# Optimization experiments

Measured on AMD Instinct MI355X. Metric: run time of the kernel, lower is better.

Reference implementation:

```python
import jax, jax.numpy as jnp
import numpy as np

N, E, H = 50000, 800000, 128
HQ = H // 4  # 32


def _mlp(x, w1, b1, w2, b2):
    return jax.nn.relu(x @ w1 + b1) @ w2 + b2


def setup_inputs() -> dict:
    key = jax.random.key(0)
    ks = jax.random.split(key, 16)

    def lin(k, fan_in, fan_out):
        lim = 1.0 / np.sqrt(fan_in)
        kw, kb = jax.random.split(k)
        w = jax.random.uniform(kw, (fan_in, fan_out), jnp.float32, -lim, lim)
        b = jax.random.uniform(kb, (fan_out,), jnp.float32, -lim, lim)
        return w, b

    x = jax.random.normal(ks[0], (N, H), jnp.float32)
    pos = jax.random.normal(ks[1], (N, 3), jnp.float32)
    edge_index = jax.random.randint(ks[2], (2, E), 0, N, jnp.int64)

    pw1, pb1 = lin(ks[3], 3, HQ)
    pw2, pb2 = lin(ks[4], HQ, HQ)
    mw1, mb1 = lin(ks[5], 2 * H + HQ, H)
    mw2, mb2 = lin(ks[6], H, H)
    uw1, ub1 = lin(ks[7], 2 * H, H)
    uw2, ub2 = lin(ks[8], H, H)

    return dict(x=x, pos=pos, edge_index=edge_index,
                pw1=pw1, pb1=pb1, pw2=pw2, pb2=pb2,
                mw1=mw1, mb1=mb1, mw2=mw2, mb2=mb2,
                uw1=uw1, ub1=ub1, uw2=uw2, ub2=ub2)


def reference(x, pos, edge_index,
              pw1, pb1, pw2, pb2,
              mw1, mb1, mw2, mb2,
              uw1, ub1, uw2, ub2):
    row, col = edge_index[0], edge_index[1]
    # position features from relative positions [E, 3] -> [E, H//4]
    pos_feat = _mlp(pos[row] - pos[col], pw1, pb1, pw2, pb2)
    # per-edge messages [E, 2H + H//4] -> [E, H]
    msg_in = jnp.concatenate([x[row], x[col], pos_feat], axis=-1)
    messages = _mlp(msg_in, mw1, mb1, mw2, mb2)
    # scatter-add messages into destination nodes (index_add on col)
    agg = jax.ops.segment_sum(messages, col, num_segments=x.shape[0])
    # node update [N, 2H] -> [N, H]
    return _mlp(jnp.concatenate([x, agg], axis=-1), uw1, ub1, uw2, ub2)
```

## Files before the change

### kernel.cpp

```cpp
#include <hip/hip_runtime.h>
#include <hip/hip_bf16.h>

#define NN 50000
#define NE 800000
#define HD 128
#define SCAN_CHUNK 1024
#define SCAN_BLOCKS ((NN + SCAN_CHUNK - 1) / SCAN_CHUNK)

typedef __attribute__((ext_vector_type(8))) short s16x8;
typedef __attribute__((ext_vector_type(4))) float f32x4;

static __device__ __forceinline__ unsigned short f2bf(float f) {
    unsigned int u = __float_as_uint(f);
    u = (u + 0x7FFFu + ((u >> 16) & 1u)) >> 16;
    return (unsigned short)u;
}
static __device__ __forceinline__ float bf2f(unsigned short h) {
    return __uint_as_float(((unsigned int)h) << 16);
}
static __device__ __forceinline__ unsigned int f2bf2(float lo, float hi) {
    __hip_bfloat162 h = __float22bfloat162_rn(make_float2(lo, hi));
    return *reinterpret_cast<unsigned int*>(&h);
}

#define WFENCE() do { asm volatile("s_waitcnt lgkmcnt(0)" ::: "memory"); \
                      __builtin_amdgcn_sched_barrier(0); } while (0)

__global__ void prep_kernel(const float* __restrict__ pw2, const float* __restrict__ pb2,
                            const float* __restrict__ mw1, const float* __restrict__ mb1,
                            float* __restrict__ Wpc, float* __restrict__ bc)
{
    int tid = threadIdx.x;
    for (int idx = tid; idx < 32 * 128; idx += 256) {
        int j = idx >> 7, k = idx & 127;
        float s = 0.f;
        #pragma unroll 8
        for (int i = 0; i < 32; ++i) s += pw2[j * 32 + i] * mw1[(256 + i) * 128 + k];
        Wpc[idx] = s;
    }
    if (tid < 128) {
        float s = mb1[tid];
        #pragma unroll 8
        for (int i = 0; i < 32; ++i) s += pb2[i] * mw1[(256 + i) * 128 + tid];
        bc[tid] = s;
    }
}

__global__ void prep2_kernel(const float* __restrict__ mw2, const float* __restrict__ mb2,
                             const float* __restrict__ uw1,
                             float* __restrict__ W3, float* __restrict__ b3)
{
    int idx = blockIdx.x * 256 + threadIdx.x;
    if (idx < 128 * 128) {
        int k = idx >> 7, j = idx & 127;
        float s = 0.f;
        #pragma unroll 4
        for (int c = 0; c < 128; ++c)
            s += mw2[k * 128 + c] * uw1[(128 + c) * 128 + j];
        W3[idx] = s;
    }
    if (blockIdx.x == 0 && threadIdx.x < 128) {
        int j = threadIdx.x;
        float s = 0.f;
        #pragma unroll 4
        for (int c = 0; c < 128; ++c)
            s += mb2[c] * uw1[(128 + c) * 128 + j];
        b3[j] = s;
    }
}

__global__ void hist_kernel(const int* __restrict__ ei, int* __restrict__ cnt)
{
    __shared__ int sIdx64;
    if (threadIdx.x == 0) {
        int z = 1;
        for (int k = 0; k < 16; ++k) if (ei[2 * k + 1] != 0) z = 0;
        sIdx64 = z;
    }
    __syncthreads();
    int g = blockIdx.x * 256 + threadIdx.x;
    if (g >= NE / 2) return;
    int e0 = g * 2;
    int c0, c1;
    if (sIdx64) { int4 q = *(const int4*)&ei[2 * NE + 2 * e0]; c0 = q.x; c1 = q.z; }
    else        { int2 q = *(const int2*)&ei[NE + e0];         c0 = q.x; c1 = q.y; }
    atomicAdd(&cnt[c0], 1);
    atomicAdd(&cnt[c1], 1);
}

__global__ void scan1_kernel(const int* __restrict__ cnt, int* __restrict__ cursor,
                             int* __restrict__ bsum)
{
    __shared__ int tot[256];
    int b = blockIdx.x, t = threadIdx.x;
    int i0 = b * SCAN_CHUNK + t * 4;
    int v[4];
    #pragma unroll
    for (int k = 0; k < 4; ++k) v[k] = (i0 + k < NN) ? cnt[i0 + k] : 0;
    tot[t] = v[0] + v[1] + v[2] + v[3];
    __syncthreads();
    if (t == 0) {
        int run = 0;
        for (int i = 0; i < 256; ++i) { int x = tot[i]; tot[i] = run; run += x; }
        bsum[b] = run;
    }
    __syncthreads();
    int p = tot[t];
    #pragma unroll
    for (int k = 0; k < 4; ++k) {
        if (i0 + k < NN) cursor[i0 + k] = p;
        p += v[k];
    }
}

__global__ void scan2_kernel(int* __restrict__ bsum)
{
    if (threadIdx.x == 0) {
        int run = 0;
        for (int i = 0; i < SCAN_BLOCKS; ++i) { int x = bsum[i]; bsum[i] = run; run += x; }
    }
}

__global__ void scan3_kernel(int* __restrict__ cursor, const int* __restrict__ bsum)
{
    int b = blockIdx.x, t = threadIdx.x;
    int carry = bsum[b];
    int i0 = b * SCAN_CHUNK + t * 4;
    #pragma unroll
    for (int k = 0; k < 4; ++k)
        if (i0 + k < NN) cursor[i0 + k] += carry;
}

__global__ void scatter_kernel(const int* __restrict__ ei,
                               int* __restrict__ cursor, int2* __restrict__ sRC)
{
    __shared__ int sIdx64;
    if (threadIdx.x == 0) {
        int z = 1;
        for (int k = 0; k < 16; ++k) if (ei[2 * k + 1] != 0) z = 0;
        sIdx64 = z;
    }
    __syncthreads();
    int g = blockIdx.x * 256 + threadIdx.x;
    if (g >= NE / 2) return;
    int e0 = g * 2;
    int r0, r1, c0, c1;
    if (sIdx64) {
        int4 qr = *(const int4*)&ei[2 * e0];           r0 = qr.x; r1 = qr.z;
        int4 qc = *(const int4*)&ei[2 * NE + 2 * e0];  c0 = qc.x; c1 = qc.z;
    } else {
        int2 qr = *(const int2*)&ei[e0];       r0 = qr.x; r1 = qr.y;
        int2 qc = *(const int2*)&ei[NE + e0];  c0 = qc.x; c1 = qc.y;
    }
    int p0 = atomicAdd(&cursor[c0], 1);
    sRC[p0] = make_int2(r0, c0);
    int p1 = atomicAdd(&cursor[c1], 1);
    sRC[p1] = make_int2(r1, c1);
}

__global__ __launch_bounds__(256, 3) void node_a_kernel(
    const float* __restrict__ x, const float* __restrict__ mw1,
    unsigned short* __restrict__ xa)
{
    __shared__ __align__(16) unsigned short sB[128 * 136];
    __shared__ __align__(16) unsigned short sSt[4][16 * 132];

    int tid = threadIdx.x;
    for (int idx = tid; idx < 128 * 128; idx += 256) {
        int c = idx & 127, k = idx >> 7;
        sB[c * 136 + k] = f2bf(mw1[k * 128 + c]);
    }
    __syncthreads();

    int lane = tid & 63, wv = tid >> 6;
    int r16 = lane & 15, g4 = lane >> 4;
    unsigned short* st = sSt[wv];
    const int NT = NN / 16;

    for (int t = blockIdx.x * 4 + wv; t < NT; t += gridDim.x * 4) {
        int r0 = t * 16;
        int row = r0 + r16;
        s16x8 a[4];
        #pragma unroll
        for (int ks = 0; ks < 4; ++ks) {
            const float* p = &x[(size_t)row * HD + ks * 32 + g4 * 8];
            float4 v0 = *(const float4*)p;
            float4 v1 = *(const float4*)(p + 4);
            union { s16x8 v; unsigned int u[4]; } av;
            av.u[0] = f2bf2(v0.x, v0.y); av.u[1] = f2bf2(v0.z, v0.w);
            av.u[2] = f2bf2(v1.x, v1.y); av.u[3] = f2bf2(v1.z, v1.w);
            a[ks] = av.v;
        }
        float hold[4];
        #pragma unroll
        for (int tc = 0; tc < 8; ++tc) {
            int col = tc * 16 + r16;
            f32x4 acc = {0.f, 0.f, 0.f, 0.f};
            #pragma unroll
            for (int ks = 0; ks < 4; ++ks) {
                s16x8 b = *(const s16x8*)&sB[col * 136 + ks * 32 + g4 * 8];
                acc = __builtin_amdgcn_mfma_f32_16x16x32_bf16(a[ks], b, acc, 0, 0, 0);
            }
            if ((tc & 1) == 0) {
                #pragma unroll
                for (int j = 0; j < 4; ++j) hold[j] = acc[j];
            } else {
                #pragma unroll
                for (int j = 0; j < 4; ++j)
                    *(unsigned int*)&st[(g4 * 4 + j) * 132 + r16 * 8 + (tc - 1)] =
                        f2bf2(hold[j], acc[j]);
            }
        }
        WFENCE();
        #pragma unroll
        for (int i = 0; i < 4; ++i) {
            int idx = i * 512 + lane * 8;
            int rr = idx >> 7, cc = idx & 127;
            *(s16x8*)&xa[(size_t)(r0 + rr) * HD + cc] = *(const s16x8*)&st[rr * 132 + cc];
        }
        WFENCE();
    }
}

__global__ __launch_bounds__(256, 3) void node_b_kernel(
    const float* __restrict__ x, const float* __restrict__ mw1,
    const float* __restrict__ bcv,
    unsigned short* __restrict__ xb)
{
    __shared__ __align__(16) unsigned short sB[128 * 136];
    __shared__ __align__(16) unsigned short sSt[4][16 * 132];

    int tid = threadIdx.x;
    for (int idx = tid; idx < 128 * 128; idx += 256) {
        int c = idx & 127, k = idx >> 7;
        sB[c * 136 + k] = f2bf(mw1[(128 + k) * 128 + c]);
    }
    __syncthreads();

    int lane = tid & 63, wv = tid >> 6;
    int r16 = lane & 15, g4 = lane >> 4;
    unsigned short* st = sSt[wv];
    float bcr[8];
    #pragma unroll
    for (int tc = 0; tc < 8; ++tc) bcr[tc] = bcv[tc * 16 + r16];
    const int NT = NN / 16;

    for (int t = blockIdx.x * 4 + wv; t < NT; t += gridDim.x * 4) {
        int r0 = t * 16;
        int row = r0 + r16;
        s16x8 a[4];
        #pragma unroll
        for (int ks = 0; ks < 4; ++ks) {
            const float* p = &x[(size_t)row * HD + ks * 32 + g4 * 8];
            float4 v0 = *(const float4*)p;
            float4 v1 = *(const float4*)(p + 4);
            union { s16x8 v; unsigned int u[4]; } av;
            av.u[0] = f2bf2(v0.x, v0.y); av.u[1] = f2bf2(v0.z, v0.w);
            av.u[2] = f2bf2(v1.x, v1.y); av.u[3] = f2bf2(v1.z, v1.w);
            a[ks] = av.v;
        }
        float hold[4];
        #pragma unroll
        for (int tc = 0; tc < 8; ++tc) {
            int col = tc * 16 + r16;
            float bv = bcr[tc];
            f32x4 acc = {bv, bv, bv, bv};
            #pragma unroll
            for (int ks = 0; ks < 4; ++ks) {
                s16x8 b = *(const s16x8*)&sB[col * 136 + ks * 32 + g4 * 8];
                acc = __builtin_amdgcn_mfma_f32_16x16x32_bf16(a[ks], b, acc, 0, 0, 0);
            }
            if ((tc & 1) == 0) {
                #pragma unroll
                for (int j = 0; j < 4; ++j) hold[j] = acc[j];
            } else {
                #pragma unroll
                for (int j = 0; j < 4; ++j)
                    *(unsigned int*)&st[(g4 * 4 + j) * 132 + r16 * 8 + (tc - 1)] =
                        f2bf2(hold[j], acc[j]);
            }
        }
        WFENCE();
        #pragma unroll
        for (int i = 0; i < 4; ++i) {
            int idx = i * 512 + lane * 8;
            int rr = idx >> 7, cc = idx & 127;
            *(s16x8*)&xb[(size_t)(r0 + rr) * HD + cc] = *(const s16x8*)&st[rr * 132 + cc];
        }
        WFENCE();
    }
}

__global__ __launch_bounds__(256, 3) void edge_kernel(
    const float* __restrict__ pos, const int2* __restrict__ sRC,
    const float* __restrict__ pw1, const float* __restrict__ pb1,
    const unsigned short* __restrict__ xa, const unsigned short* __restrict__ xb,
    const float* __restrict__ Wpc,
    float* __restrict__ aggH)
{
    __shared__ __align__(16) unsigned short sT[4][16 * 136];
    __shared__ int sECs[4][16];

    int tid = threadIdx.x;
    int lane = tid & 63, wv = tid >> 6;
    int r16 = lane & 15, g4 = lane >> 4;
    unsigned short* stg = sT[wv];
    int* secw = sECs[wv];

    s16x8 wr[8];
    #pragma unroll
    for (int tc = 0; tc < 8; ++tc) {
        s16x8 w;
        #pragma unroll
        for (int i = 0; i < 8; ++i)
            w[i] = (short)f2bf(Wpc[(g4 * 8 + i) * 128 + tc * 16 + r16]);
        wr[tc] = w;
    }
    float pw10[8], pw11[8], pw12[8], pb1r[8];
    #pragma unroll
    for (int i = 0; i < 8; ++i) {
        int k = g4 * 8 + i;
        pw10[i] = pw1[k]; pw11[i] = pw1[32 + k]; pw12[i] = pw1[64 + k];
        pb1r[i] = pb1[k];
    }

    const int NW = gridDim.x * 4;
    const int NT = NE / 16;
    int gw = blockIdx.x * 4 + wv;
    if (gw >= NT) return;

    int2 rc = sRC[gw * 16 + r16];
    int2 rcN = rc;
    if (gw + NW < NT) rcN = sRC[(gw + NW) * 16 + r16];
    float dp0 = pos[rc.x * 3 + 0] - pos[rc.y * 3 + 0];
    float dp1 = pos[rc.x * 3 + 1] - pos[rc.y * 3 + 1];
    float dp2 = pos[rc.x * 3 + 2] - pos[rc.y * 3 + 2];
    s16x8 ga[4], gb[4];
    #pragma unroll
    for (int j = 0; j < 4; ++j) {
        int gx = __shfl(rc.x, g4 * 4 + j, 64);
        int gy = __shfl(rc.y, g4 * 4 + j, 64);
        ga[j] = *(const s16x8*)&xa[(size_t)gx * HD + r16 * 8];
        gb[j] = *(const s16x8*)&xb[(size_t)gy * HD + r16 * 8];
    }

    for (int t = gw; t < NT; t += NW) {
        bool hn  = (t + NW) < NT;
        bool hn2 = (t + 2 * NW) < NT;

        if (lane < 16) secw[lane] = rc.y;
        union { s16x8 v; unsigned int u[4]; } apf;
        #pragma unroll
        for (int i2 = 0; i2 < 4; ++i2) {
            int i = 2 * i2;
            float v0 = fmaf(dp0, pw10[i], fmaf(dp1, pw11[i], fmaf(dp2, pw12[i], pb1r[i])));
            float v1 = fmaf(dp0, pw10[i+1], fmaf(dp1, pw11[i+1], fmaf(dp2, pw12[i+1], pb1r[i+1])));
            apf.u[i2] = f2bf2(fmaxf(v0, 0.f), fmaxf(v1, 0.f));
        }

        float hold[4];
        #pragma unroll
        for (int tc = 0; tc < 8; ++tc) {
            f32x4 acc;
            #pragma unroll
            for (int j = 0; j < 4; ++j)
                acc[j] = bf2f((unsigned short)ga[j][tc]) + bf2f((unsigned short)gb[j][tc]);
            acc = __builtin_amdgcn_mfma_f32_16x16x32_bf16(apf.v, wr[tc], acc, 0, 0, 0);
            if ((tc & 1) == 0) {
                #pragma unroll
                for (int j = 0; j < 4; ++j) hold[j] = fmaxf(acc[j], 0.f);
            } else {
                #pragma unroll
                for (int j = 0; j < 4; ++j)
                    *(unsigned int*)&stg[(g4 * 4 + j) * 136 + r16 * 8 + (tc - 1)] =
                        f2bf2(hold[j], fmaxf(acc[j], 0.f));
            }
        }
        WFENCE();

        if (hn) {
            #pragma unroll
            for (int j = 0; j < 4; ++j) {
                int gx = __shfl(rcN.x, g4 * 4 + j, 64);
                int gy = __shfl(rcN.y, g4 * 4 + j, 64);
                ga[j] = *(const s16x8*)&xa[(size_t)gx * HD + r16 * 8];
                gb[j] = *(const s16x8*)&xb[(size_t)gy * HD + r16 * 8];
            }
        }

        int2 rcN2 = rcN;
        if (hn2) rcN2 = sRC[(t + 2 * NW) * 16 + r16];
        float dp0N = 0.f, dp1N = 0.f, dp2N = 0.f;
        if (hn) {
            dp0N = pos[rcN.x * 3 + 0] - pos[rcN.y * 3 + 0];
            dp1N = pos[rcN.x * 3 + 1] - pos[rcN.y * 3 + 1];
            dp2N = pos[rcN.x * 3 + 2] - pos[rcN.y * 3 + 2];
        }

        {
            int p0 = (lane & 15) * 8 + (lane >> 4);
            int p1 = p0 + 4;
            int cur = secw[0];
            float run0 = bf2f(stg[p0]);
            float run1 = bf2f(stg[p1]);
            #pragma unroll
            for (int e = 1; e < 16; ++e) {
                int c = secw[e];
                float v0 = bf2f(stg[e * 136 + p0]);
                float v1 = bf2f(stg[e * 136 + p1]);
                if (c != cur) {
                    unsafeAtomicAdd(&aggH[(size_t)cur * HD + lane], run0);
                    unsafeAtomicAdd(&aggH[(size_t)cur * HD + lane + 64], run1);
                    cur = c; run0 = v0; run1 = v1;
                } else { run0 += v0; run1 += v1; }
            }
            unsafeAtomicAdd(&aggH[(size_t)cur * HD + lane], run0);
            unsafeAtomicAdd(&aggH[(size_t)cur * HD + lane + 64], run1);
        }
        WFENCE();

        rc = rcN; rcN = rcN2; dp0 = dp0N; dp1 = dp1N; dp2 = dp2N;
    }
}

__global__ __launch_bounds__(512, 2) void upd_kernel(
    const float* __restrict__ x, const float* __restrict__ aggH,
    const int* __restrict__ cnt,
    const float* __restrict__ uw1, const float* __restrict__ ub1,
    const float* __restrict__ W3, const float* __restrict__ b3,
    const float* __restrict__ uw2, const float* __restrict__ ub2,
    float* __restrict__ out)
{
    __shared__ __align__(16) unsigned short sB1a[128 * 136];
    __shared__ __align__(16) unsigned short sW3l[128 * 136];
    __shared__ __align__(16) unsigned short sB2[128 * 136];
    __shared__ __align__(16) unsigned short sSt[8][16 * 136];

    int tid = threadIdx.x;
    for (int idx = tid; idx < 128 * 128; idx += 512) {
        int c = idx & 127, k = idx >> 7;
        sB1a[c * 136 + k] = f2bf(uw1[k * 128 + c]);
        sW3l[c * 136 + k] = f2bf(W3[k * 128 + c]);
        sB2[c * 136 + k]  = f2bf(uw2[k * 128 + c]);
    }
    __syncthreads();

    int lane = tid & 63, wv = tid >> 6;
    int r16 = lane & 15, g4 = lane >> 4;
    unsigned short* st = sSt[wv];
    float ub1r[8], ub2r[8], b3r[8];
    #pragma unroll
    for (int tc = 0; tc < 8; ++tc) {
        ub1r[tc] = ub1[tc * 16 + r16];
        ub2r[tc] = ub2[tc * 16 + r16];
        b3r[tc]  = b3[tc * 16 + r16];
    }

    const int NT = NN / 16;
    for (int t = blockIdx.x * 8 + wv; t < NT; t += gridDim.x * 8) {
        int r0 = t * 16;
        int row = r0 + r16;
        s16x8 a[8];
        #pragma unroll
        for (int ks = 0; ks < 8; ++ks) {
            const float* p = (ks < 4) ? &x[(size_t)row * HD + ks * 32 + g4 * 8]
                                      : &aggH[(size_t)row * HD + (ks - 4) * 32 + g4 * 8];
            float4 v0 = *(const float4*)p;
            float4 v1 = *(const float4*)(p + 4);
            union { s16x8 v; unsigned int u[4]; } av;
            av.u[0] = f2bf2(v0.x, v0.y); av.u[1] = f2bf2(v0.z, v0.w);
            av.u[2] = f2bf2(v1.x, v1.y); av.u[3] = f2bf2(v1.z, v1.w);
            a[ks] = av.v;
        }
        float cn[4];
        #pragma unroll
        for (int j = 0; j < 4; ++j) cn[j] = (float)cnt[r0 + g4 * 4 + j];

        #pragma unroll
        for (int tc = 0; tc < 8; ++tc) {
            int col = tc * 16 + r16;
            f32x4 acc;
            #pragma unroll
            for (int j = 0; j < 4; ++j) acc[j] = ub1r[tc] + cn[j] * b3r[tc];
            #pragma unroll
            for (int ks = 0; ks < 4; ++ks) {
                s16x8 b = *(const s16x8*)&sB1a[col * 136 + ks * 32 + g4 * 8];
                acc = __builtin_amdgcn_mfma_f32_16x16x32_bf16(a[ks], b, acc, 0, 0, 0);
            }
            #pragma unroll
            for (int ks = 4; ks < 8; ++ks) {
                s16x8 b = *(const s16x8*)&sW3l[col * 136 + (ks - 4) * 32 + g4 * 8];
                acc = __builtin_amdgcn_mfma_f32_16x16x32_bf16(a[ks], b, acc, 0, 0, 0);
            }
            #pragma unroll
            for (int j = 0; j < 4; ++j)
                st[(g4 * 4 + j) * 136 + col] = f2bf(fmaxf(acc[j], 0.f));
        }
        WFENCE();
        s16x8 a2[4];
        #pragma unroll
        for (int ks = 0; ks < 4; ++ks)
            a2[ks] = *(const s16x8*)&st[r16 * 136 + ks * 32 + g4 * 8];
        WFENCE();
        #pragma unroll
        for (int tc = 0; tc < 8; ++tc) {
            int col = tc * 16 + r16;
            float bv = ub2r[tc];
            f32x4 acc = {bv, bv, bv, bv};
            #pragma unroll
            for (int ks = 0; ks < 4; ++ks) {
                s16x8 b = *(const s16x8*)&sB2[col * 136 + ks * 32 + g4 * 8];
                acc = __builtin_amdgcn_mfma_f32_16x16x32_bf16(a2[ks], b, acc, 0, 0, 0);
            }
            #pragma unroll
            for (int j = 0; j < 4; ++j)
                out[(size_t)(r0 + g4 * 4 + j) * HD + col] = acc[j];
        }
    }
}

extern "C" void kernel_launch(void* const* d_in, const int* in_sizes, int n_in,
                              void* d_out, int out_size, void* d_ws, size_t ws_size,
                              hipStream_t stream)
{
    const float* x   = (const float*)d_in[0];
    const float* pos = (const float*)d_in[1];
    const int*   ei  = (const int*)d_in[2];
    const float* pw1 = (const float*)d_in[3];
    const float* pb1 = (const float*)d_in[4];
    const float* pw2 = (const float*)d_in[5];
    const float* pb2 = (const float*)d_in[6];
    const float* mw1 = (const float*)d_in[7];
    const float* mb1 = (const float*)d_in[8];
    const float* mw2 = (const float*)d_in[9];
    const float* mb2 = (const float*)d_in[10];
    const float* uw1 = (const float*)d_in[11];
    const float* ub1 = (const float*)d_in[12];
    const float* uw2 = (const float*)d_in[13];
    const float* ub2 = (const float*)d_in[14];
    float* out = (float*)d_out;

    char* ws = (char*)d_ws;
    float*          aggH   = (float*)(ws);
    unsigned short* xa     = (unsigned short*)(ws + 25600000);
    unsigned short* xb     = (unsigned short*)(ws + 38400000);
    float*          Wpc    = (float*)(ws + 51200000);
    float*          bcv    = (float*)(ws + 51216384);
    int*            cnt    = (int*)(ws + 51216896);
    int*            cursor = (int*)(ws + 51417600);
    int*            bsum   = (int*)(ws + 51618304);
    int2*           sRC    = (int2*)(ws + 51618560);

    float* W3 = (float*)(ws + 51417600);
    float* b3 = (float*)(ws + 51417600 + 65536);

    hipMemsetAsync(aggH, 0, (size_t)NN * HD * sizeof(float), stream);
    hipMemsetAsync(cnt, 0, NN * sizeof(int), stream);
    prep_kernel<<<1, 256, 0, stream>>>(pw2, pb2, mw1, mb1, Wpc, bcv);
    hist_kernel<<<(NE / 2 + 255) / 256, 256, 0, stream>>>(ei, cnt);
    scan1_kernel<<<SCAN_BLOCKS, 256, 0, stream>>>(cnt, cursor, bsum);
    scan2_kernel<<<1, 64, 0, stream>>>(bsum);
    scan3_kernel<<<SCAN_BLOCKS, 256, 0, stream>>>(cursor, bsum);
    scatter_kernel<<<(NE / 2 + 255) / 256, 256, 0, stream>>>(ei, cursor, sRC);
    prep2_kernel<<<64, 256, 0, stream>>>(mw2, mb2, uw1, W3, b3);
    node_a_kernel<<<512, 256, 0, stream>>>(x, mw1, xa);
    node_b_kernel<<<512, 256, 0, stream>>>(x, mw1, bcv, xb);
    edge_kernel<<<768, 256, 0, stream>>>(pos, sRC, pw1, pb1, xa, xb, Wpc, aggH);
    upd_kernel<<<256, 512, 0, stream>>>(x, aggH, cnt, uw1, ub1, W3, b3, uw2, ub2, out);
}
```

Before: 244.1 us.

## Merge prep, scan and node kernels; fold aggH zeroing into node kernel

Merges the two weight-prep kernels into one launch and removes the single-thread scan2 kernel, so each scan3 block now sums the earlier block totals itself. The two node projection kernels become one launch in which block parity selects the weight half and the output buffer, and that kernel also zeroes aggH in place of the separate memset. The update kernel grows to 768 threads with 12 waves per block. The aim is fewer launches and less serialization between small kernels. The risks are lower occupancy in upd_kernel, a larger LDS footprint, and repeated reads of bsum across scan3 blocks.

```diff
diff --git a/kernel.cpp b/kernel.cpp
--- a/kernel.cpp
+++ b/kernel.cpp
@@ -25,49 +25,6 @@
 
 #define WFENCE() do { asm volatile("s_waitcnt lgkmcnt(0)" ::: "memory"); \
                       __builtin_amdgcn_sched_barrier(0); } while (0)
-
-__global__ void prep_kernel(const float* __restrict__ pw2, const float* __restrict__ pb2,
-                            const float* __restrict__ mw1, const float* __restrict__ mb1,
-                            float* __restrict__ Wpc, float* __restrict__ bc)
-{
-    int tid = threadIdx.x;
-    for (int idx = tid; idx < 32 * 128; idx += 256) {
-        int j = idx >> 7, k = idx & 127;
-        float s = 0.f;
-        #pragma unroll 8
-        for (int i = 0; i < 32; ++i) s += pw2[j * 32 + i] * mw1[(256 + i) * 128 + k];
-        Wpc[idx] = s;
-    }
-    if (tid < 128) {
-        float s = mb1[tid];
-        #pragma unroll 8
-        for (int i = 0; i < 32; ++i) s += pb2[i] * mw1[(256 + i) * 128 + tid];
-        bc[tid] = s;
-    }
-}
-
-__global__ void prep2_kernel(const float* __restrict__ mw2, const float* __restrict__ mb2,
-                             const float* __restrict__ uw1,
-                             float* __restrict__ W3, float* __restrict__ b3)
-{
-    int idx = blockIdx.x * 256 + threadIdx.x;
-    if (idx < 128 * 128) {
-        int k = idx >> 7, j = idx & 127;
-        float s = 0.f;
-        #pragma unroll 4
-        for (int c = 0; c < 128; ++c)
-            s += mw2[k * 128 + c] * uw1[(128 + c) * 128 + j];
-        W3[idx] = s;
-    }
-    if (blockIdx.x == 0 && threadIdx.x < 128) {
-        int j = threadIdx.x;
-        float s = 0.f;
-        #pragma unroll 4
-        for (int c = 0; c < 128; ++c)
-            s += mb2[c] * uw1[(128 + c) * 128 + j];
-        b3[j] = s;
-    }
-}
 
 __global__ void hist_kernel(const int* __restrict__ ei, int* __restrict__ cnt)
 {
@@ -113,18 +70,17 @@
     }
 }
 
-__global__ void scan2_kernel(int* __restrict__ bsum)
-{
-    if (threadIdx.x == 0) {
+__global__ void scan3_kernel(int* __restrict__ cursor, const int* __restrict__ bsum)
+{
+    __shared__ int sCarry;
+    int b = blockIdx.x, t = threadIdx.x;
+    if (t == 0) {
         int run = 0;
-        for (int i = 0; i < SCAN_BLOCKS; ++i) { int x = bsum[i]; bsum[i] = run; run += x; }
-    }
-}
-
-__global__ void scan3_kernel(int* __restrict__ cursor, const int* __restrict__ bsum)
-{
-    int b = blockIdx.x, t = threadIdx.x;
-    int carry = bsum[b];
+        for (int i = 0; i < b; ++i) run += bsum[i];
+        sCarry = run;
+    }
+    __syncthreads();
+    int carry = sCarry;
     int i0 = b * SCAN_CHUNK + t * 4;
     #pragma unroll
     for (int k = 0; k < 4; ++k)
@@ -158,26 +114,84 @@
     sRC[p1] = make_int2(r1, c1);
 }
 
-__global__ __launch_bounds__(256, 3) void node_a_kernel(
+__global__ void prepall_kernel(const float* __restrict__ pw2, const float* __restrict__ pb2,
+                               const float* __restrict__ mw1, const float* __restrict__ mb1,
+                               const float* __restrict__ mw2, const float* __restrict__ mb2,
+                               const float* __restrict__ uw1,
+                               float* __restrict__ Wpc, float* __restrict__ bc,
+                               float* __restrict__ W3, float* __restrict__ b3)
+{
+    int tid = threadIdx.x;
+    if (blockIdx.x == 64) {
+        for (int idx = tid; idx < 32 * 128; idx += 256) {
+            int j = idx >> 7, k = idx & 127;
+            float s = 0.f;
+            #pragma unroll 8
+            for (int i = 0; i < 32; ++i) s += pw2[j * 32 + i] * mw1[(256 + i) * 128 + k];
+            Wpc[idx] = s;
+        }
+        if (tid < 128) {
+            float s = mb1[tid];
+            #pragma unroll 8
+            for (int i = 0; i < 32; ++i) s += pb2[i] * mw1[(256 + i) * 128 + tid];
+            bc[tid] = s;
+        }
+        return;
+    }
+    int idx = blockIdx.x * 256 + tid;
+    {
+        int k = idx >> 7, j = idx & 127;
+        float s = 0.f;
+        #pragma unroll 4
+        for (int c = 0; c < 128; ++c)
+            s += mw2[k * 128 + c] * uw1[(128 + c) * 128 + j];
+        W3[idx] = s;
+    }
+    if (blockIdx.x == 0 && tid < 128) {
+        int j = tid;
+        float s = 0.f;
+        #pragma unroll 4
+        for (int c = 0; c < 128; ++c)
+            s += mb2[c] * uw1[(128 + c) * 128 + j];
+        b3[j] = s;
+    }
+}
+
+__global__ __launch_bounds__(256, 3) void node_kernel(
     const float* __restrict__ x, const float* __restrict__ mw1,
-    unsigned short* __restrict__ xa)
+    const float* __restrict__ bcv,
+    unsigned short* __restrict__ xa, unsigned short* __restrict__ xb,
+    float* __restrict__ aggH)
 {
     __shared__ __align__(16) unsigned short sB[128 * 136];
     __shared__ __align__(16) unsigned short sSt[4][16 * 132];
 
     int tid = threadIdx.x;
+    {
+        f32x4 z = {0.f, 0.f, 0.f, 0.f};
+        const int total4 = NN * HD / 4;
+        for (int i = blockIdx.x * 256 + tid; i < total4; i += gridDim.x * 256)
+            ((f32x4*)aggH)[i] = z;
+    }
+    int half = blockIdx.x & 1;
     for (int idx = tid; idx < 128 * 128; idx += 256) {
         int c = idx & 127, k = idx >> 7;
-        sB[c * 136 + k] = f2bf(mw1[k * 128 + c]);
+        sB[c * 136 + k] = f2bf(mw1[(half * 128 + k) * 128 + c]);
     }
     __syncthreads();
 
     int lane = tid & 63, wv = tid >> 6;
     int r16 = lane & 15, g4 = lane >> 4;
     unsigned short* st = sSt[wv];
+    unsigned short* dst = half ? xb : xa;
+    float bcr[8];
+    #pragma unroll
+    for (int tc = 0; tc < 8; ++tc) bcr[tc] = half ? bcv[tc * 16 + r16] : 0.f;
     const int NT = NN / 16;
-
-    for (int t = blockIdx.x * 4 + wv; t < NT; t += gridDim.x * 4) {
+    const int nb = gridDim.x >> 1;
+    const int bid = blockIdx.x >> 1;
+
+    for (int t = bid * 4 + wv; t < NT; t += nb * 4) {
         int r0 = t * 16;
         int row = r0 + r16;
         s16x8 a[4];
@@ -195,7 +209,8 @@
         #pragma unroll
         for (int tc = 0; tc < 8; ++tc) {
             int col = tc * 16 + r16;
-            f32x4 acc = {0.f, 0.f, 0.f, 0.f};
+            float bv = bcr[tc];
+            f32x4 acc = {bv, bv, bv, bv};
             #pragma unroll
             for (int ks = 0; ks < 4; ++ks) {
                 s16x8 b = *(const s16x8*)&sB[col * 136 + ks * 32 + g4 * 8];
@@ -216,76 +231,7 @@
         for (int i = 0; i < 4; ++i) {
             int idx = i * 512 + lane * 8;
             int rr = idx >> 7, cc = idx & 127;
-            *(s16x8*)&xa[(size_t)(r0 + rr) * HD + cc] = *(const s16x8*)&st[rr * 132 + cc];
-        }
-        WFENCE();
-    }
-}
-
-__global__ __launch_bounds__(256, 3) void node_b_kernel(
-    const float* __restrict__ x, const float* __restrict__ mw1,
-    const float* __restrict__ bcv,
-    unsigned short* __restrict__ xb)
-{
-    __shared__ __align__(16) unsigned short sB[128 * 136];
-    __shared__ __align__(16) unsigned short sSt[4][16 * 132];
-
-    int tid = threadIdx.x;
-    for (int idx = tid; idx < 128 * 128; idx += 256) {
-        int c = idx & 127, k = idx >> 7;
-        sB[c * 136 + k] = f2bf(mw1[(128 + k) * 128 + c]);
-    }
-    __syncthreads();
-
-    int lane = tid & 63, wv = tid >> 6;
-    int r16 = lane & 15, g4 = lane >> 4;
-    unsigned short* st = sSt[wv];
-    float bcr[8];
-    #pragma unroll
-    for (int tc = 0; tc < 8; ++tc) bcr[tc] = bcv[tc * 16 + r16];
-    const int NT = NN / 16;
-
-    for (int t = blockIdx.x * 4 + wv; t < NT; t += gridDim.x * 4) {
-        int r0 = t * 16;
-        int row = r0 + r16;
-        s16x8 a[4];
-        #pragma unroll
-        for (int ks = 0; ks < 4; ++ks) {
-            const float* p = &x[(size_t)row * HD + ks * 32 + g4 * 8];
-            float4 v0 = *(const float4*)p;
-            float4 v1 = *(const float4*)(p + 4);
-            union { s16x8 v; unsigned int u[4]; } av;
-            av.u[0] = f2bf2(v0.x, v0.y); av.u[1] = f2bf2(v0.z, v0.w);
-            av.u[2] = f2bf2(v1.x, v1.y); av.u[3] = f2bf2(v1.z, v1.w);
-            a[ks] = av.v;
-        }
-        float hold[4];
-        #pragma unroll
-        for (int tc = 0; tc < 8; ++tc) {
-            int col = tc * 16 + r16;
-            float bv = bcr[tc];
-            f32x4 acc = {bv, bv, bv, bv};
-            #pragma unroll
-            for (int ks = 0; ks < 4; ++ks) {
-                s16x8 b = *(const s16x8*)&sB[col * 136 + ks * 32 + g4 * 8];
-                acc = __builtin_amdgcn_mfma_f32_16x16x32_bf16(a[ks], b, acc, 0, 0, 0);
-            }
-            if ((tc & 1) == 0) {
-                #pragma unroll
-                for (int j = 0; j < 4; ++j) hold[j] = acc[j];
-            } else {
-                #pragma unroll
-                for (int j = 0; j < 4; ++j)
-                    *(unsigned int*)&st[(g4 * 4 + j) * 132 + r16 * 8 + (tc - 1)] =
-                        f2bf2(hold[j], acc[j]);
-            }
-        }
-        WFENCE();
-        #pragma unroll
-        for (int i = 0; i < 4; ++i) {
-            int idx = i * 512 + lane * 8;
-            int rr = idx >> 7, cc = idx & 127;
-            *(s16x8*)&xb[(size_t)(r0 + rr) * HD + cc] = *(const s16x8*)&st[rr * 132 + cc];
+            *(s16x8*)&dst[(size_t)(r0 + rr) * HD + cc] = *(const s16x8*)&st[rr * 132 + cc];
         }
         WFENCE();
     }
@@ -423,7 +369,7 @@
     }
 }
 
-__global__ __launch_bounds__(512, 2) void upd_kernel(
+__global__ __launch_bounds__(768, 1) void upd_kernel(
     const float* __restrict__ x, const float* __restrict__ aggH,
     const int* __restrict__ cnt,
     const float* __restrict__ uw1, const float* __restrict__ ub1,
@@ -434,10 +380,10 @@
     __shared__ __align__(16) unsigned short sB1a[128 * 136];
     __shared__ __align__(16) unsigned short sW3l[128 * 136];
     __shared__ __align__(16) unsigned short sB2[128 * 136];
-    __shared__ __align__(16) unsigned short sSt[8][16 * 136];
+    __shared__ __align__(16) unsigned short sSt[12][16 * 136];
 
     int tid = threadIdx.x;
-    for (int idx = tid; idx < 128 * 128; idx += 512) {
+    for (int idx = tid; idx < 128 * 128; idx += 768) {
         int c = idx & 127, k = idx >> 7;
         sB1a[c * 136 + k] = f2bf(uw1[k * 128 + c]);
         sW3l[c * 136 + k] = f2bf(W3[k * 128 + c]);
@@ -457,7 +403,7 @@
     }
 
     const int NT = NN / 16;
-    for (int t = blockIdx.x * 8 + wv; t < NT; t += gridDim.x * 8) {
+    for (int t = blockIdx.x * 12 + wv; t < NT; t += gridDim.x * 12) {
         int r0 = t * 16;
         int row = r0 + r16;
         s16x8 a[8];
@@ -554,17 +500,14 @@
     float* W3 = (float*)(ws + 51417600);
     float* b3 = (float*)(ws + 51417600 + 65536);
 
-    hipMemsetAsync(aggH, 0, (size_t)NN * HD * sizeof(float), stream);
     hipMemsetAsync(cnt, 0, NN * sizeof(int), stream);
-    prep_kernel<<<1, 256, 0, stream>>>(pw2, pb2, mw1, mb1, Wpc, bcv);
     hist_kernel<<<(NE / 2 + 255) / 256, 256, 0, stream>>>(ei, cnt);
     scan1_kernel<<<SCAN_BLOCKS, 256, 0, stream>>>(cnt, cursor, bsum);
-    scan2_kernel<<<1, 64, 0, stream>>>(bsum);
     scan3_kernel<<<SCAN_BLOCKS, 256, 0, stream>>>(cursor, bsum);
     scatter_kernel<<<(NE / 2 + 255) / 256, 256, 0, stream>>>(ei, cursor, sRC);
-    prep2_kernel<<<64, 256, 0, stream>>>(mw2, mb2, uw1, W3, b3);
-    node_a_kernel<<<512, 256, 0, stream>>>(x, mw1, xa);
-    node_b_kernel<<<512, 256, 0, stream>>>(x, mw1, bcv, xb);
+    prepall_kernel<<<65, 256, 0, stream>>>(pw2, pb2, mw1, mb1, mw2, mb2, uw1,
+                                           Wpc, bcv, W3, b3);
+    node_kernel<<<1024, 256, 0, stream>>>(x, mw1, bcv, xa, xb, aggH);
     edge_kernel<<<768, 256, 0, stream>>>(pos, sRC, pw1, pb1, xa, xb, Wpc, aggH);
-    upd_kernel<<<256, 512, 0, stream>>>(x, aggH, cnt, uw1, ub1, W3, b3, uw2, ub2, out);
-}
+    upd_kernel<<<256, 768, 0, stream>>>(x, aggH, cnt, uw1, ub1, W3, b3, uw2, ub2, out);
+}
```

Result: faster. 229.7 us (-5.9%).
